# Optimization experiments

Measured on AMD Instinct MI355X. Metric: run time of the kernel, lower is better.

Reference implementation:

```python
import jax, jax.numpy as jnp
import numpy as np

EPSILON = 10.0
N_ITERS = 10
TOL = 1e-06
N, DIM = 8192, 128


def setup_inputs() -> dict:
    key = jax.random.key(0)
    kx, ky = jax.random.split(key)
    x = jax.random.normal(kx, (N, DIM), dtype=jnp.float32)
    y = jax.random.normal(ky, (N, DIM), dtype=jnp.float32)
    return {"x": x, "y": y}


def _sinkhorn_plan(C):
    # uniform marginals, as in the torch module defaults
    n = C.shape[0]
    a = jnp.full((n,), 1.0 / n, dtype=C.dtype)
    b = a
    K = jnp.exp(-C / EPSILON)  # [n, n]
    u0 = jnp.ones((n,), dtype=C.dtype)
    v0 = jnp.ones((n,), dtype=C.dtype)

    def step(carry, _):
        u, v, done = carry
        u_new = a / (K @ v)
        v_new = b / (K.T @ u_new)
        # torch breaks AFTER applying the update, so the converging step is kept
        conv = jnp.linalg.norm(u_new - u) < TOL
        u = jnp.where(done, u, u_new)
        v = jnp.where(done, v, v_new)
        return (u, v, done | conv), None

    (u, v, _), _ = jax.lax.scan(step, (u0, v0, jnp.array(False)), None, length=N_ITERS)
    # diag(u) @ K @ diag(v) == u[:,None] * K * v[None,:] (no diag materialization)
    return u[:, None] * K * v[None, :]


def reference(x, y):
    # torch.cdist(x, y, p=2): pairwise L2 distances [n, n]
    x2 = jnp.sum(x * x, axis=1)
    y2 = jnp.sum(y * y, axis=1)
    d2 = x2[:, None] + y2[None, :] - 2.0 * (x @ y.T)
    C = jnp.sqrt(jnp.maximum(d2, 0.0))

    P = _sinkhorn_plan(C)
    transport_cost = jnp.sum(P * C)
    entropy = -jnp.sum(P * jnp.log(P + 1e-09))
    divergence = transport_cost + EPSILON * entropy
    return divergence, P
```

## Files before the change

kernel.cpp:

```cpp
#include <hip/hip_runtime.h>

#define N 8192
#define DIM 128
#define EPS 10.0f
#define AINV (1.0f / 8192.0f)
#define C1 (-0.14426950408889634f)

typedef __attribute__((ext_vector_type(8))) short short8;
typedef __attribute__((ext_vector_type(4))) float f32x4;

static __device__ __forceinline__ unsigned short f2bf(float f) {
  unsigned int b = __float_as_uint(f);
  unsigned int lsb = (b >> 16) & 1u;
  b += 0x7fffu + lsb;
  return (unsigned short)(b >> 16);
}

static __device__ __forceinline__ void stage16k(const uint4* __restrict__ g, uint4* l,
                                                int wid, int lane) {
#pragma unroll
  for (int s = 0; s < 4; ++s) {
    int base = wid * 256 + s * 64;
    __builtin_amdgcn_global_load_lds(
        (const __attribute__((address_space(1))) void*)(g + base + lane),
        (__attribute__((address_space(3))) void*)(l + base), 16, 0, 0);
  }
}

__global__ __launch_bounds__(256) void k_convert(const float* __restrict__ x, const float* __restrict__ y,
                                                 unsigned short* __restrict__ xb, unsigned short* __restrict__ yb,
                                                 float* __restrict__ x2, float* __restrict__ y2,
                                                 float* __restrict__ u, float* __restrict__ vpartB,
                                                 float* __restrict__ normp, double* __restrict__ accs) {
  int r = blockIdx.x * 4 + (threadIdx.x >> 6);
  int l = threadIdx.x & 63;
  const float* src = (r < N) ? (x + (size_t)r * DIM) : (y + (size_t)(r - N) * DIM);
  float2 f = ((const float2*)src)[l];
  unsigned short* dst = (r < N) ? (xb + (size_t)r * DIM) : (yb + (size_t)(r - N) * DIM);
  ushort2 h; h.x = f2bf(f.x); h.y = f2bf(f.y);
  int di = (((l >> 2) ^ (r & 7)) << 2) | (l & 3);
  ((ushort2*)dst)[di] = h;
  float s = f.x * f.x + f.y * f.y;
#pragma unroll
  for (int off = 32; off >= 1; off >>= 1) s += __shfl_down(s, off);
  if (l == 0) { if (r < N) x2[r] = s; else y2[r - N] = s; }
  if (r < N) {
    if (l == 0) { u[r] = 1.f; vpartB[r] = AINV; }
    else if (l < 16) vpartB[(size_t)l * N + r] = 0.f;
  }
  if (r == 0) {
    normp[l] = 1e30f;
    if (l < 16) normp[64 + l] = 1e30f;
    if (l == 0) { accs[0] = 0.0; accs[1] = 0.0; }
  }
}

__global__ __launch_bounds__(256, 3) void k_pass(const unsigned short* __restrict__ Ab,
                                                 const unsigned short* __restrict__ Bb,
                                                 const float* __restrict__ a2, const float* __restrict__ b2,
                                                 const float* __restrict__ wpart,
                                                 float* __restrict__ outpart,
                                                 float* __restrict__ u_arr,
                                                 float* __restrict__ normp,
                                                 int t, int write_norm) {
  for (int tt = 0; tt < t; ++tt) {
    float s = 0.f;
#pragma unroll
    for (int q = 0; q < 8; ++q) s += normp[tt * 8 + q];
    if (s < 1e-12f) return;
  }
  __shared__ uint4 buf[2][1024];
  __shared__ float wv_lds[1024];
  __shared__ float b2_lds[1024];
  __shared__ float red[256];
  const int jc = blockIdx.x;
  const int ic = blockIdx.y;
  const int i0 = ic * 128;
  const int tid = threadIdx.x;
  const int wid = tid >> 6, lane = tid & 63;
  const uint4* ag = (const uint4*)Ab + (size_t)i0 * 16;
  const uint4* bwin = (const uint4*)Bb + (size_t)jc * 1024 * 16;
  stage16k(bwin, buf[0], wid, lane);
  const int wr = (wid >> 1) * 64, wc = (wid & 1) * 32;
  const int lhi = lane >> 4, llo = lane & 15;
  short8 afr[4][4];
#pragma unroll
  for (int kk = 0; kk < 4; ++kk)
#pragma unroll
    for (int m = 0; m < 4; ++m) {
      int rx = wr + m * 16 + llo;
      afr[kk][m] = *(const short8*)(ag + rx * 16 + ((kk * 4 + lhi) ^ (rx & 7)));
    }
  float a2v[4][4], rsum[4][4];
#pragma unroll
  for (int m = 0; m < 4; ++m)
#pragma unroll
    for (int r = 0; r < 4; ++r) {
      a2v[m][r] = a2[i0 + wr + m * 16 + lhi * 4 + r];
      rsum[m][r] = 0.f;
    }
  {
    const float4* wp4 = (const float4*)wpart;
    int w4 = jc * 256 + tid;
    float4 s4 = wp4[w4];
#pragma unroll
    for (int q = 1; q < 16; ++q) {
      float4 p = wp4[(size_t)q * 2048 + w4];
      s4.x += p.x; s4.y += p.y; s4.z += p.z; s4.w += p.w;
    }
    float4 wn;
    wn.x = AINV * __builtin_amdgcn_rcpf(s4.x);
    wn.y = AINV * __builtin_amdgcn_rcpf(s4.y);
    wn.z = AINV * __builtin_amdgcn_rcpf(s4.z);
    wn.w = AINV * __builtin_amdgcn_rcpf(s4.w);
    ((float4*)wv_lds)[tid] = wn;
    ((float4*)b2_lds)[tid] = ((const float4*)b2)[w4];
    if (write_norm && ic == 0) {
      float4 uo = ((const float4*)u_arr)[w4];
      float dd = (wn.x - uo.x) * (wn.x - uo.x) + (wn.y - uo.y) * (wn.y - uo.y) +
                 (wn.z - uo.z) * (wn.z - uo.z) + (wn.w - uo.w) * (wn.w - uo.w);
      ((float4*)u_arr)[w4] = wn;
      red[tid] = dd;
      __syncthreads();
      for (int st = 128; st > 0; st >>= 1) {
        if (tid < st) red[tid] += red[tid + st];
        __syncthreads();
      }
      if (tid == 0) normp[t * 8 + jc] = red[0];
    }
  }
  __syncthreads();
  for (int sc = 0; sc < 16; ++sc) {
    if (sc < 15) stage16k(bwin + (sc + 1) * 1024, buf[(sc + 1) & 1], wid, lane);
    const uint4* bs = buf[sc & 1];
    float wv[2], b2v[2];
#pragma unroll
    for (int n = 0; n < 2; ++n) {
      int jl = sc * 64 + wc + n * 16 + llo;
      wv[n] = wv_lds[jl];
      b2v[n] = b2_lds[jl];
    }
    f32x4 acc[4][2];
    f32x4 zero = {0.f, 0.f, 0.f, 0.f};
#pragma unroll
    for (int m = 0; m < 4; ++m)
#pragma unroll
      for (int n = 0; n < 2; ++n) acc[m][n] = zero;
#pragma unroll
    for (int kk = 0; kk < 4; ++kk) {
      short8 bfr[2];
#pragma unroll
      for (int n = 0; n < 2; ++n) {
        int ry = wc + n * 16 + llo;
        bfr[n] = *(const short8*)&bs[ry * 16 + ((kk * 4 + lhi) ^ (ry & 7))];
      }
#pragma unroll
      for (int m = 0; m < 4; ++m)
#pragma unroll
        for (int n = 0; n < 2; ++n)
          acc[m][n] = __builtin_amdgcn_mfma_f32_16x16x32_bf16(afr[kk][m], bfr[n], acc[m][n], 0, 0, 0);
    }
#pragma unroll
    for (int m = 0; m < 4; ++m)
#pragma unroll
      for (int n = 0; n < 2; ++n)
#pragma unroll
        for (int r = 0; r < 4; ++r) {
          float d2 = fmaf(-2.f, acc[m][n][r], a2v[m][r] + b2v[n]);
          float c = __builtin_amdgcn_sqrtf(fmaxf(d2, 0.f));
          rsum[m][r] = fmaf(__builtin_amdgcn_exp2f(c * C1), wv[n], rsum[m][r]);
        }
    __syncthreads();
  }
#pragma unroll
  for (int m = 0; m < 4; ++m)
#pragma unroll
    for (int r = 0; r < 4; ++r) {
      float s = rsum[m][r];
      s += __shfl_xor(s, 1);
      s += __shfl_xor(s, 2);
      s += __shfl_xor(s, 4);
      s += __shfl_xor(s, 8);
      rsum[m][r] = s;
    }
  if (llo == 0) {
    float* vp = outpart + (size_t)(jc * 2 + (wid & 1)) * N;
#pragma unroll
    for (int m = 0; m < 4; ++m)
#pragma unroll
      for (int r = 0; r < 4; ++r)
        vp[i0 + wr + m * 16 + lhi * 4 + r] = rsum[m][r];
  }
}

__global__ __launch_bounds__(256) void k_final(const unsigned short* __restrict__ xb,
                                               const unsigned short* __restrict__ yb,
                                               const float* __restrict__ x2, const float* __restrict__ y2,
                                               const float* __restrict__ u, const float* __restrict__ vpartB,
                                               float* __restrict__ D, double* __restrict__ accs) {
  __shared__ uint4 xs[128 * 16];
  __shared__ uint4 ys[128 * 16];
  __shared__ float vv_lds[128];
  const int i0 = blockIdx.y * 128;
  const int j0 = blockIdx.x * 128;
  const int tid = threadIdx.x;
  const uint4* xg = (const uint4*)xb + (size_t)i0 * 16;
  const uint4* yg = (const uint4*)yb + (size_t)j0 * 16;
#pragma unroll
  for (int s = 0; s < 8; ++s) {
    int q = tid + s * 256;
    xs[q] = xg[q];
    ys[q] = yg[q];
  }
  if (tid < 32) {
    const float4* vp4 = (const float4*)vpartB;
    int w4 = (j0 >> 2) + tid;
    float4 s4 = vp4[w4];
#pragma unroll
    for (int q = 1; q < 16; ++q) {
      float4 p = vp4[(size_t)q * 2048 + w4];
      s4.x += p.x; s4.y += p.y; s4.z += p.z; s4.w += p.w;
    }
    float4 vn;
    vn.x = AINV * __builtin_amdgcn_rcpf(s4.x);
    vn.y = AINV * __builtin_amdgcn_rcpf(s4.y);
    vn.z = AINV * __builtin_amdgcn_rcpf(s4.z);
    vn.w = AINV * __builtin_amdgcn_rcpf(s4.w);
    ((float4*)vv_lds)[tid] = vn;
  }
  __syncthreads();
  const int wid = tid >> 6, lane = tid & 63;
  const int wr = (wid >> 1) * 64, wc = (wid & 1) * 64;
  const int lhi = lane >> 4, llo = lane & 15;
  float x2v[4][4], uvv[4][4], y2v[4], vv[4];
#pragma unroll
  for (int m = 0; m < 4; ++m)
#pragma unroll
    for (int r = 0; r < 4; ++r) {
      int i = i0 + wr + m * 16 + lhi * 4 + r;
      x2v[m][r] = x2[i];
      uvv[m][r] = u[i];
    }
#pragma unroll
  for (int n = 0; n < 4; ++n) {
    int j = j0 + wc + n * 16 + llo;
    y2v[n] = y2[j];
    vv[n] = vv_lds[wc + n * 16 + llo];
  }
  f32x4 acc[4][4];
  f32x4 zero = {0.f, 0.f, 0.f, 0.f};
#pragma unroll
  for (int m = 0; m < 4; ++m)
#pragma unroll
    for (int n = 0; n < 4; ++n) acc[m][n] = zero;
#pragma unroll
  for (int kk = 0; kk < 4; ++kk) {
    short8 af[4], bfr[4];
#pragma unroll
    for (int m = 0; m < 4; ++m) {
      int rx = wr + m * 16 + llo;
      af[m] = *(const short8*)&xs[rx * 16 + ((kk * 4 + lhi) ^ (rx & 7))];
      int ry = wc + m * 16 + llo;
      bfr[m] = *(const short8*)&ys[ry * 16 + ((kk * 4 + lhi) ^ (ry & 7))];
    }
#pragma unroll
    for (int m = 0; m < 4; ++m)
#pragma unroll
      for (int n = 0; n < 4; ++n)
        acc[m][n] = __builtin_amdgcn_mfma_f32_16x16x32_bf16(af[m], bfr[n], acc[m][n], 0, 0, 0);
  }
  float lc = 0.f, le = 0.f;
#pragma unroll
  for (int m = 0; m < 4; ++m) {
#pragma unroll
    for (int n = 0; n < 4; ++n) {
#pragma unroll
      for (int r = 0; r < 4; ++r) {
        int i = i0 + wr + m * 16 + lhi * 4 + r;
        int j = j0 + wc + n * 16 + llo;
        float d2 = fmaf(-2.f, acc[m][n][r], x2v[m][r] + y2v[n]);
        float c = __builtin_amdgcn_sqrtf(fmaxf(d2, 0.f));
        float k = __builtin_amdgcn_exp2f(c * C1);
        float p = uvv[m][r] * k * vv[n];
        D[1 + (size_t)i * N + j] = p;
        lc = fmaf(p, c, lc);
        le = fmaf(p, __logf(p + 1e-9f), le);
      }
    }
  }
  __syncthreads();
  double* r0 = (double*)xs;
  double* r1 = r0 + 256;
  r0[tid] = (double)lc;
  r1[tid] = (double)le;
  __syncthreads();
  for (int s = 128; s > 0; s >>= 1) {
    if (tid < s) {
      r0[tid] += r0[tid + s];
      r1[tid] += r1[tid + s];
    }
    __syncthreads();
  }
  if (tid == 0) {
    atomicAdd(&accs[0], r0[0]);
    atomicAdd(&accs[1], r1[0]);
  }
}

__global__ void k_write_div(float* D, const double* accs) {
  if (threadIdx.x == 0 && blockIdx.x == 0)
    D[0] = (float)(accs[0] - (double)EPS * accs[1]);
}

extern "C" void kernel_launch(void* const* d_in, const int* in_sizes, int n_in,
                              void* d_out, int out_size, void* d_ws, size_t ws_size,
                              hipStream_t stream) {
  const float* x = (const float*)d_in[0];
  const float* y = (const float*)d_in[1];
  float* D = (float*)d_out;
  char* w = (char*)d_ws;
  unsigned short* xb = (unsigned short*)w;
  unsigned short* yb = (unsigned short*)(w + 2097152);
  float* fb = (float*)(w + 4194304);
  float* x2 = fb;
  float* y2 = fb + 8192;
  float* u = fb + 16384;
  float* vpartA = fb + 24576;
  float* vpartB = vpartA + 16 * N;
  float* normp = vpartB + 16 * N;
  double* accs = (double*)(normp + 96);

  k_convert<<<4096, 256, 0, stream>>>(x, y, xb, yb, x2, y2, u, vpartB, normp, accs);
  for (int it = 0; it < 4; ++it) {
    k_pass<<<dim3(8, 64), 256, 0, stream>>>(xb, yb, x2, y2, vpartB, vpartA, u, normp, it, 0);
    k_pass<<<dim3(8, 64), 256, 0, stream>>>(yb, xb, y2, x2, vpartA, vpartB, u, normp, it, 1);
  }
  k_final<<<dim3(64, 64), 256, 0, stream>>>(xb, yb, x2, y2, u, vpartB, D, accs);
  k_write_div<<<1, 64, 0, stream>>>(D, accs);
}
```

Measured before the change: 261.4 us.

## Read B fragments directly from global, fold exp scale into sqrt, nontemporal P stores

The Sinkhorn pass kernel stops staging B tiles into LDS with async global_load_lds double buffering. It now reads the bf16 fragments directly from global memory (L2/cache), which also removes the per-chunk barrier. The constant 1/(eps·ln2) is folded into the squared-distance terms (scaled by C1SQ) so the inner loop drops one multiply before exp2. The final plan writes use nontemporal stores to avoid polluting the cache. Direct global fragment loads risk higher latency and possible uncoalesced access compared with the LDS path.

```diff
diff --git a/kernel.cpp b/kernel.cpp
--- a/kernel.cpp
+++ b/kernel.cpp
@@ -5,6 +5,7 @@
 #define EPS 10.0f
 #define AINV (1.0f / 8192.0f)
 #define C1 (-0.14426950408889634f)
+#define C1SQ (0.020813712f)
 
 typedef __attribute__((ext_vector_type(8))) short short8;
 typedef __attribute__((ext_vector_type(4))) float f32x4;
@@ -14,17 +15,6 @@
   unsigned int lsb = (b >> 16) & 1u;
   b += 0x7fffu + lsb;
   return (unsigned short)(b >> 16);
-}
-
-static __device__ __forceinline__ void stage16k(const uint4* __restrict__ g, uint4* l,
-                                                int wid, int lane) {
-#pragma unroll
-  for (int s = 0; s < 4; ++s) {
-    int base = wid * 256 + s * 64;
-    __builtin_amdgcn_global_load_lds(
-        (const __attribute__((address_space(1))) void*)(g + base + lane),
-        (__attribute__((address_space(3))) void*)(l + base), 16, 0, 0);
-  }
 }
 
 __global__ __launch_bounds__(256) void k_convert(const float* __restrict__ x, const float* __restrict__ y,
@@ -69,7 +59,6 @@
     for (int q = 0; q < 8; ++q) s += normp[tt * 8 + q];
     if (s < 1e-12f) return;
   }
-  __shared__ uint4 buf[2][1024];
   __shared__ float wv_lds[1024];
   __shared__ float b2_lds[1024];
   __shared__ float red[256];
@@ -80,7 +69,6 @@
   const int wid = tid >> 6, lane = tid & 63;
   const uint4* ag = (const uint4*)Ab + (size_t)i0 * 16;
   const uint4* bwin = (const uint4*)Bb + (size_t)jc * 1024 * 16;
-  stage16k(bwin, buf[0], wid, lane);
   const int wr = (wid >> 1) * 64, wc = (wid & 1) * 32;
   const int lhi = lane >> 4, llo = lane & 15;
   short8 afr[4][4];
@@ -96,7 +84,7 @@
   for (int m = 0; m < 4; ++m)
 #pragma unroll
     for (int r = 0; r < 4; ++r) {
-      a2v[m][r] = a2[i0 + wr + m * 16 + lhi * 4 + r];
+      a2v[m][r] = a2[i0 + wr + m * 16 + lhi * 4 + r] * C1SQ;
       rsum[m][r] = 0.f;
     }
   {
@@ -114,7 +102,9 @@
     wn.z = AINV * __builtin_amdgcn_rcpf(s4.z);
     wn.w = AINV * __builtin_amdgcn_rcpf(s4.w);
     ((float4*)wv_lds)[tid] = wn;
-    ((float4*)b2_lds)[tid] = ((const float4*)b2)[w4];
+    float4 b4 = ((const float4*)b2)[w4];
+    b4.x *= C1SQ; b4.y *= C1SQ; b4.z *= C1SQ; b4.w *= C1SQ;
+    ((float4*)b2_lds)[tid] = b4;
     if (write_norm && ic == 0) {
       float4 uo = ((const float4*)u_arr)[w4];
       float dd = (wn.x - uo.x) * (wn.x - uo.x) + (wn.y - uo.y) * (wn.y - uo.y) +
@@ -131,8 +121,6 @@
   }
   __syncthreads();
   for (int sc = 0; sc < 16; ++sc) {
-    if (sc < 15) stage16k(bwin + (sc + 1) * 1024, buf[(sc + 1) & 1], wid, lane);
-    const uint4* bs = buf[sc & 1];
     float wv[2], b2v[2];
 #pragma unroll
     for (int n = 0; n < 2; ++n) {
@@ -151,8 +139,8 @@
       short8 bfr[2];
 #pragma unroll
       for (int n = 0; n < 2; ++n) {
-        int ry = wc + n * 16 + llo;
-        bfr[n] = *(const short8*)&bs[ry * 16 + ((kk * 4 + lhi) ^ (ry & 7))];
+        int rw = sc * 64 + wc + n * 16 + llo;
+        bfr[n] = *(const short8*)(bwin + (size_t)rw * 16 + ((kk * 4 + lhi) ^ (llo & 7)));
       }
 #pragma unroll
       for (int m = 0; m < 4; ++m)
@@ -166,11 +154,10 @@
       for (int n = 0; n < 2; ++n)
 #pragma unroll
         for (int r = 0; r < 4; ++r) {
-          float d2 = fmaf(-2.f, acc[m][n][r], a2v[m][r] + b2v[n]);
-          float c = __builtin_amdgcn_sqrtf(fmaxf(d2, 0.f));
-          rsum[m][r] = fmaf(__builtin_amdgcn_exp2f(c * C1), wv[n], rsum[m][r]);
+          float tt = fmaf(-2.f * C1SQ, acc[m][n][r], a2v[m][r] + b2v[n]);
+          float ss = __builtin_amdgcn_sqrtf(fmaxf(tt, 0.f));
+          rsum[m][r] = fmaf(__builtin_amdgcn_exp2f(-ss), wv[n], rsum[m][r]);
         }
-    __syncthreads();
   }
 #pragma unroll
   for (int m = 0; m < 4; ++m)
@@ -282,7 +269,7 @@
         float c = __builtin_amdgcn_sqrtf(fmaxf(d2, 0.f));
         float k = __builtin_amdgcn_exp2f(c * C1);
         float p = uvv[m][r] * k * vv[n];
-        D[1 + (size_t)i * N + j] = p;
+        __builtin_nontemporal_store(p, &D[1 + (size_t)i * N + j]);
         lc = fmaf(p, c, lc);
         le = fmaf(p, __logf(p + 1e-9f), le);
       }
```

Result: slower. 353.2 us (+35.1%).
